# Performance work log

Hardware: AMD Instinct MI355X
Metric: run time of the kernel (lower is better)

The kernel has to match this reference:

```python
import jax, jax.numpy as jnp
import numpy as np

TWO_PI = 2.0 * 3.14159  # matches the torch source constant exactly
N_RINGS = 5
N_ORIENT = 8


def setup_inputs() -> dict:
    key = jax.random.key(0)
    k1, k2, k3 = jax.random.split(key, 3)
    B, N, CIN, COUT = 4, 32768, 32, 32
    features = jax.random.normal(k1, (B, N, CIN), dtype=jnp.float32)
    # radial in [0,1), angular in [0, 2*pi)
    coords01 = jax.random.uniform(k2, (B, N, 2), dtype=jnp.float32)
    geodesic_coords = coords01 * jnp.array([1.0, TWO_PI], dtype=jnp.float32)
    filters = jax.random.normal(k3, (N_RINGS, N_ORIENT, CIN, COUT), dtype=jnp.float32) * 0.01
    bias = jnp.zeros((COUT,), dtype=jnp.float32)
    return {"features": features, "geodesic_coords": geodesic_coords,
            "filters": filters, "bias": bias}


def reference(features, geodesic_coords, filters, bias):
    radial = geodesic_coords[:, :, 0]
    angular = geodesic_coords[:, :, 1]
    # torch .long() truncates toward zero; values are non-negative so astype matches
    ring_idx = jnp.clip((radial * N_RINGS).astype(jnp.int32), 0, N_RINGS - 1)
    orient_idx = jnp.clip((angular * N_ORIENT / TWO_PI).astype(jnp.int32), 0, N_ORIENT - 1)
    # gather per-point filter matrix: (B, N, Cin, Cout)
    W = filters[ring_idx, orient_idx]
    out = jnp.einsum('bnc,bncd->bnd', features, W) + bias
    return out
```

## Files before the change

kernel.cpp:

```cpp
#include <hip/hip_runtime.h>


#define NPTS_PER_BLOCK 64
#define THREADS 256

__global__ __launch_bounds__(THREADS, 4)
void geodesic_conv_kernel(const float* __restrict__ feat,
                          const float* __restrict__ coords,
                          const float* __restrict__ filt,
                          const float* __restrict__ bias,
                          float* __restrict__ out)
{
    __shared__ float4 lds_f4[NPTS_PER_BLOCK * 8];
    __shared__ int    lds_bin[NPTS_PER_BLOCK];

    const int tid   = threadIdx.x;
    const int pbase = blockIdx.x * NPTS_PER_BLOCK;

    const float4* gf4 = reinterpret_cast<const float4*>(feat) + (size_t)pbase * 8;
    lds_f4[tid]       = gf4[tid];
    lds_f4[tid + 256] = gf4[tid + 256];

    if (tid < NPTS_PER_BLOCK) {
        float2 rc = reinterpret_cast<const float2*>(coords)[pbase + tid];
        int ri = (int)(rc.x * 5.0f);
        ri = min(max(ri, 0), 4);
        const float TWO_PI_F = (float)(2.0 * 3.14159);
        int oi = (int)((rc.y * 8.0f) / TWO_PI_F);
        oi = min(max(oi, 0), 7);
        lds_bin[tid] = ri * 8 + oi;
    }
    __syncthreads();

    const int wave = tid >> 6;
    const int lane = tid & 63;
    const int half = lane >> 5;
    const int d    = lane & 31;
    const float bs = bias[d];

    for (int i = 0; i < 8; ++i) {
        const int p   = wave * 16 + i * 2 + half;
        const int bin = lds_bin[p];
        const float* W = filt + (size_t)bin * 1024 + d;
        float acc = 0.0f;
        #pragma unroll
        for (int c4 = 0; c4 < 8; ++c4) {
            float4 fv = lds_f4[p * 8 + c4];
            acc += fv.x * W[(c4 * 4 + 0) * 32];
            acc += fv.y * W[(c4 * 4 + 1) * 32];
            acc += fv.z * W[(c4 * 4 + 2) * 32];
            acc += fv.w * W[(c4 * 4 + 3) * 32];
        }
        out[(size_t)(pbase + p) * 32 + d] = acc + bs;
    }
}

extern "C" void kernel_launch(void* const* d_in, const int* in_sizes, int n_in,
                              void* d_out, int out_size, void* d_ws, size_t ws_size,
                              hipStream_t stream) {
    const float* feat   = (const float*)d_in[0];
    const float* coords = (const float*)d_in[1];
    const float* filt   = (const float*)d_in[2];
    const float* bias   = (const float*)d_in[3];
    float* out = (float*)d_out;

    const int npts    = in_sizes[0] / 32;
    const int nblocks = npts / NPTS_PER_BLOCK;
    geodesic_conv_kernel<<<nblocks, THREADS, 0, stream>>>(feat, coords, filt, bias, out);
}
```

Measured before the change: 88.55 us.

## Rewrite geodesic conv as per-bin masked bf16 MFMA with LDS-staged filters

Replaces the scalar FP32 per-point dot-product kernel with one that converts all 40 filter bins to bf16 and stages them in LDS for each 1024-thread block. Each wave takes 32 points, finds the distinct bins among them with ballots, and for each bin runs 16x16x32 bf16 MFMAs on feature rows masked to that bin. This moves the work onto the matrix cores and removes scattered global filter reads, but it lowers precision to bf16 and makes every block repeat the full filter conversion. A wave can loop over up to 32 distinct bins, so much of the matrix work is done on masked-out rows.

New measurement: 80.87 us. 8.7% less time.

```diff
diff --git a/kernel.cpp b/kernel.cpp
--- a/kernel.cpp
+++ b/kernel.cpp
@@ -1,70 +1,127 @@
 #include <hip/hip_runtime.h>
 
 
-#define NPTS_PER_BLOCK 64
-#define THREADS 256
+#define NBINS 40
+#define THREADS 1024
+#define PTS_BLK 512
+
+typedef __attribute__((ext_vector_type(8))) short bf16x8;
+typedef __attribute__((ext_vector_type(4))) float f32x4;
+
+__device__ __forceinline__ unsigned short f2bf(float x) {
+    unsigned u = __float_as_uint(x);
+    u += 0x7FFFu + ((u >> 16) & 1u);
+    return (unsigned short)(u >> 16);
+}
+
+__device__ __forceinline__ int bin_of(float2 rc) {
+    const float TWO_PI_F = (float)(2.0 * 3.14159);
+    int ri = (int)(rc.x * 5.0f);
+    ri = min(max(ri, 0), 4);
+    int oi = (int)((rc.y * 8.0f) / TWO_PI_F);
+    oi = min(max(oi, 0), 7);
+    return ri * 8 + oi;
+}
 
 __global__ __launch_bounds__(THREADS, 4)
-void geodesic_conv_kernel(const float* __restrict__ feat,
-                          const float* __restrict__ coords,
-                          const float* __restrict__ filt,
-                          const float* __restrict__ bias,
-                          float* __restrict__ out)
-{
-    __shared__ float4 lds_f4[NPTS_PER_BLOCK * 8];
-    __shared__ int    lds_bin[NPTS_PER_BLOCK];
+void k_fused(const float* __restrict__ feat, const float2* __restrict__ coords,
+             const float* __restrict__ filt, const float* __restrict__ bias,
+             float* __restrict__ out) {
+    __shared__ __align__(16) unsigned short Wl[NBINS * 2 * 64 * 8];
+    __shared__ int wlist[16][32];
 
-    const int tid   = threadIdx.x;
-    const int pbase = blockIdx.x * NPTS_PER_BLOCK;
+    const int tid  = threadIdx.x;
+    const int lane = tid & 63;
+    const int wave = tid >> 6;
+    const int l15  = lane & 15;
+    const int kg   = lane >> 4;
+    const int pbase = blockIdx.x * PTS_BLK + wave * 32;
 
-    const float4* gf4 = reinterpret_cast<const float4*>(feat) + (size_t)pbase * 8;
-    lds_f4[tid]       = gf4[tid];
-    lds_f4[tid + 256] = gf4[tid + 256];
+    for (int it = tid; it < NBINS * 128; it += THREADS) {
+        const int il = it & 15, ik = (it >> 4) & 3, in = (it >> 6) & 1, ib = it >> 7;
+        const float* src = filt + ib * 1024 + ik * 256 + in * 16 + il;
+        bf16x8 w;
+        #pragma unroll
+        for (int j = 0; j < 8; ++j) w[j] = (short)f2bf(src[j * 32]);
+        *reinterpret_cast<bf16x8*>(&Wl[it * 8]) = w;
+    }
 
-    if (tid < NPTS_PER_BLOCK) {
-        float2 rc = reinterpret_cast<const float2*>(coords)[pbase + tid];
-        int ri = (int)(rc.x * 5.0f);
-        ri = min(max(ri, 0), 4);
-        const float TWO_PI_F = (float)(2.0 * 3.14159);
-        int oi = (int)((rc.y * 8.0f) / TWO_PI_F);
-        oi = min(max(oi, 0), 7);
-        lds_bin[tid] = ri * 8 + oi;
+    const int myb = bin_of(coords[pbase + (lane & 31)]);
+    bf16x8 af[2];
+    #pragma unroll
+    for (int m = 0; m < 2; ++m) {
+        const float* fp = feat + (size_t)(pbase + m * 16 + l15) * 32 + kg * 8;
+        const float4 v0 = *reinterpret_cast<const float4*>(fp);
+        const float4 v1 = *reinterpret_cast<const float4*>(fp + 4);
+        bf16x8 a;
+        a[0] = (short)f2bf(v0.x); a[1] = (short)f2bf(v0.y);
+        a[2] = (short)f2bf(v0.z); a[3] = (short)f2bf(v0.w);
+        a[4] = (short)f2bf(v1.x); a[5] = (short)f2bf(v1.y);
+        a[6] = (short)f2bf(v1.z); a[7] = (short)f2bf(v1.w);
+        af[m] = a;
     }
+    const int bm0 = __shfl(myb, l15);
+    const int bm1 = __shfl(myb, 16 + l15);
+
+    int cnt = 0;
+    unsigned long long rem = __ballot(1);
+    while (rem) {
+        const int src = (int)__ffsll((long long)rem) - 1;
+        const int bb  = __shfl(myb, src);
+        rem &= ~__ballot(myb == bb);
+        if (lane == 0) wlist[wave][cnt] = bb;
+        ++cnt;
+    }
+
     __syncthreads();
 
-    const int wave = tid >> 6;
-    const int lane = tid & 63;
-    const int half = lane >> 5;
-    const int d    = lane & 31;
-    const float bs = bias[d];
+    f32x4 acc[2][2];
+    {
+        const float bv0 = bias[l15];
+        const float bv1 = bias[16 + l15];
+        #pragma unroll
+        for (int m = 0; m < 2; ++m) {
+            acc[m][0] = (f32x4){bv0, bv0, bv0, bv0};
+            acc[m][1] = (f32x4){bv1, bv1, bv1, bv1};
+        }
+    }
 
-    for (int i = 0; i < 8; ++i) {
-        const int p   = wave * 16 + i * 2 + half;
-        const int bin = lds_bin[p];
-        const float* W = filt + (size_t)bin * 1024 + d;
-        float acc = 0.0f;
+    int bb = wlist[wave][0];
+    bf16x8 B0 = *reinterpret_cast<const bf16x8*>(&Wl[((bb * 2 + 0) * 64 + lane) * 8]);
+    bf16x8 B1 = *reinterpret_cast<const bf16x8*>(&Wl[((bb * 2 + 1) * 64 + lane) * 8]);
+    for (int i = 0; i < cnt; ++i) {
+        const int nx  = (i + 1 < cnt) ? i + 1 : i;
+        const int bbn = wlist[wave][nx];
+        const bf16x8 N0 = *reinterpret_cast<const bf16x8*>(&Wl[((bbn * 2 + 0) * 64 + lane) * 8]);
+        const bf16x8 N1 = *reinterpret_cast<const bf16x8*>(&Wl[((bbn * 2 + 1) * 64 + lane) * 8]);
+        bf16x8 a0 = af[0]; if (bm0 != bb) a0 = (bf16x8)0;
+        bf16x8 a1 = af[1]; if (bm1 != bb) a1 = (bf16x8)0;
+        acc[0][0] = __builtin_amdgcn_mfma_f32_16x16x32_bf16(a0, B0, acc[0][0], 0, 0, 0);
+        acc[0][1] = __builtin_amdgcn_mfma_f32_16x16x32_bf16(a0, B1, acc[0][1], 0, 0, 0);
+        acc[1][0] = __builtin_amdgcn_mfma_f32_16x16x32_bf16(a1, B0, acc[1][0], 0, 0, 0);
+        acc[1][1] = __builtin_amdgcn_mfma_f32_16x16x32_bf16(a1, B1, acc[1][1], 0, 0, 0);
+        bb = bbn; B0 = N0; B1 = N1;
+    }
+
+    #pragma unroll
+    for (int m = 0; m < 2; ++m)
         #pragma unroll
-        for (int c4 = 0; c4 < 8; ++c4) {
-            float4 fv = lds_f4[p * 8 + c4];
-            acc += fv.x * W[(c4 * 4 + 0) * 32];
-            acc += fv.y * W[(c4 * 4 + 1) * 32];
-            acc += fv.z * W[(c4 * 4 + 2) * 32];
-            acc += fv.w * W[(c4 * 4 + 3) * 32];
+        for (int r = 0; r < 4; ++r) {
+            const size_t o = (size_t)(pbase + m * 16 + kg * 4 + r) * 32;
+            out[o + l15]      = acc[m][0][r];
+            out[o + 16 + l15] = acc[m][1][r];
         }
-        out[(size_t)(pbase + p) * 32 + d] = acc + bs;
-    }
 }
 
 extern "C" void kernel_launch(void* const* d_in, const int* in_sizes, int n_in,
                               void* d_out, int out_size, void* d_ws, size_t ws_size,
                               hipStream_t stream) {
-    const float* feat   = (const float*)d_in[0];
-    const float* coords = (const float*)d_in[1];
-    const float* filt   = (const float*)d_in[2];
-    const float* bias   = (const float*)d_in[3];
+    const float*  feat   = (const float*)d_in[0];
+    const float2* coords = (const float2*)d_in[1];
+    const float*  filt   = (const float*)d_in[2];
+    const float*  bias   = (const float*)d_in[3];
     float* out = (float*)d_out;
 
-    const int npts    = in_sizes[0] / 32;
-    const int nblocks = npts / NPTS_PER_BLOCK;
-    geodesic_conv_kernel<<<nblocks, THREADS, 0, stream>>>(feat, coords, filt, bias, out);
+    const int npts = in_sizes[0] / 32;
+    k_fused<<<npts / PTS_BLK, THREADS, 0, stream>>>(feat, coords, filt, bias, out);
 }
```
